# Kernel optimization log

Measured on AMD Instinct MI355X. Metric: run time of the kernel, lower is better.

## Reference

```python
import jax, jax.numpy as jnp
import numpy as np

N_DIS = 5000
N_GEN = 20000
N = N_DIS + N_GEN
E = 400000
N_MIRNA = 2000
EMB = 128
HID = 64


def setup_inputs() -> dict:
    key = jax.random.key(0)
    ks = jax.random.split(key, 20)
    def g(k, shape, scale=0.05):
        return jax.random.normal(k, shape, dtype=jnp.float32) * scale
    return {
        'd_features': g(ks[0], (N_DIS, 383), 1.0),
        'g_features': g(ks[1], (N_GEN, 4395), 1.0),
        'miRNA_dis': jax.random.uniform(ks[2], (N_MIRNA, N_DIS), dtype=jnp.float32),
        'gene_dis': jax.random.uniform(ks[3], (N_GEN, N_DIS), dtype=jnp.float32),
        'Wd': g(ks[4], (383, EMB)),
        'bd': jnp.zeros((EMB,), jnp.float32),
        'Wg': g(ks[5], (4395, EMB)),
        'bg': jnp.zeros((EMB,), jnp.float32),
        'W1': g(ks[6], (N_MIRNA, EMB)),
        'W4': g(ks[7], (N_DIS, EMB)),
        'Ws1': g(ks[8], (EMB, HID)),
        'Wn1': g(ks[9], (EMB, HID)),
        'b1': jnp.zeros((HID,), jnp.float32),
        'Ws2': g(ks[10], (HID, HID)),
        'Wn2': g(ks[11], (HID, HID)),
        'b2': jnp.zeros((HID,), jnp.float32),
        'src': jax.random.randint(ks[12], (E,), 0, N, dtype=jnp.int32),
        'dst': jax.random.randint(ks[13], (E,), 0, N, dtype=jnp.int32),
    }


def _sage_mean(h, src, dst, Ws, Wn, b):
    # DGL SAGEConv 'mean': fc_self(h) + fc_neigh(mean over in-neighbors) + bias
    msg = h[src]                                            # [E, d] gather
    agg = jax.ops.segment_sum(msg, dst, num_segments=N)     # [N, d] scatter-add
    deg = jax.ops.segment_sum(jnp.ones((dst.shape[0],), h.dtype), dst, num_segments=N)
    neigh = agg / jnp.maximum(deg, 1.0)[:, None]            # mean (zero-deg -> 0)
    return h @ Ws + neigh @ Wn + b


def reference(d_features, g_features, miRNA_dis, gene_dis, Wd, bd, Wg, bg,
              W1, W4, Ws1, Wn1, b1, Ws2, Wn2, b2, src, dst):
    # CrossCompressUnit outputs used by forward: A2 = M1^T W1, B1 = M2 W4
    A2 = miRNA_dis.T @ W1          # [N_DIS, EMB]
    B1 = gene_dis @ W4             # [N_GEN, EMB]
    # Node embeddings (dropout is identity at inference; torch.no_grad block)
    h_dis = 0.9 * (d_features @ Wd + bd) + 0.1 * A2   # [N_DIS, EMB]
    h_gen = 0.9 * (g_features @ Wg + bg) + 0.1 * B1   # [N_GEN, EMB]
    h = jnp.concatenate([h_dis, h_gen], axis=0)        # [N, EMB]
    h = _sage_mean(h, src, dst, Ws1, Wn1, b1)          # [N, 64]
    h = jax.nn.relu(h)
    h = _sage_mean(h, src, dst, Ws2, Wn2, b2)          # [N, 64]
    return h
```

## Files before the change

### kernel.cpp

```cpp
#include <hip/hip_runtime.h>

#define NDIS 5000
#define NGEN 20000
#define NTOT 25000
#define EDG  400000

typedef __attribute__((ext_vector_type(8))) short short8;
typedef __attribute__((ext_vector_type(4))) float f32x4;
typedef __attribute__((ext_vector_type(4), aligned(4))) float f32x4u;
typedef __attribute__((ext_vector_type(4))) unsigned int uint4v;
typedef __attribute__((ext_vector_type(2))) unsigned int uint2v;
typedef __attribute__((ext_vector_type(2), aligned(4))) unsigned int uint2a;

constexpr size_t AL(size_t x) { return (x + 255) & ~(size_t)255; }
constexpr size_t OFF_H0   = 0;
constexpr size_t OFF_PQ   = AL(OFF_H0  + (size_t)NTOT * 128 * 4);
constexpr size_t OFF_H1   = AL(OFF_PQ  + (size_t)NTOT * 128 * 4);
constexpr size_t OFF_DEG  = AL(OFF_H1  + (size_t)NTOT * 128 * 4);
constexpr size_t OFF_RS   = AL(OFF_DEG + (size_t)NTOT * 4);
constexpr size_t OFF_CUR  = AL(OFF_RS  + (size_t)(NTOT + 1) * 4);
constexpr size_t OFF_ESRC = AL(OFF_CUR + (size_t)NTOT * 4);
constexpr size_t OFF_MIT  = AL(OFF_ESRC + (size_t)EDG * 4);
constexpr size_t OFF_BDIS = AL(OFF_MIT + (size_t)5000 * 2048 * 2);
constexpr size_t OFF_BGEN = AL(OFF_BDIS + (size_t)8 * 76 * 512 * 2);
constexpr size_t OFF_BS1  = AL(OFF_BGEN + (size_t)8 * 300 * 512 * 2);
constexpr size_t OFF_BS2  = AL(OFF_BS1 + (size_t)8 * 4 * 512 * 2);
constexpr size_t OFF_PD   = AL(OFF_BS2 + (size_t)8 * 4 * 512 * 2);
constexpr size_t OFF_PG   = AL(OFF_PD + (size_t)5 * NDIS * 128 * 4);

__device__ __forceinline__ ushort f2bf(float f) {
    unsigned u = __float_as_uint(f);
    u += 0x7fffu + ((u >> 16) & 1u);
    return (ushort)(u >> 16);
}

__device__ __forceinline__ unsigned cvtpk(float a, float b) {
    unsigned r;
    asm("v_cvt_pk_bf16_f32 %0, %1, %2" : "=v"(r) : "v"(a), "v"(b));
    return r;
}

__device__ __forceinline__ void MFMA(f32x4& d, short8 a, short8 b) {
    asm volatile("v_mfma_f32_16x16x32_bf16 %0, %1, %2, %0"
                 : "+v"(d) : "v"(a), "v"(b));
}

struct TcvtIns { const float* p[9]; };

__global__ __launch_bounds__(256) void k_tcvt_multi(TcvtIns ins, char* ws,
                                                    const int* __restrict__ dst,
                                                    int* __restrict__ deg)
{
    constexpr int   TR[9]   = {383, 2000, 4395, 5000, 2000, 128, 128, 64, 64};
    constexpr int   TC[9]   = {128, 128, 128, 128, 5000, 64, 64, 64, 64};
    constexpr int   TKT[9]  = {76, 76, 300, 300, 2048 , 4, 4, 4, 4};
    constexpr int   TKO[9]  = {0, 12, 0, 140, 0, 0, 0, 0, 0};
    constexpr int   TRP[9]  = {384, 2048, 4480, 5120, 2048, 128, 128, 128, 128};
    constexpr int   TNOFF[9]= {0, 0, 0, 0, 0, 0, 64, 0, 64};
    constexpr int   TMODE[9]= {1, 1, 1, 1, 0, 1, 1, 1, 1};
    constexpr float TSC[9]  = {0.9f, 0.1f, 0.9f, 0.1f, 1.f, 1.f, 1.f, 1.f, 1.f};
    constexpr size_t TOUT[9]= {OFF_BDIS, OFF_BDIS, OFF_BGEN, OFF_BGEN, OFF_MIT,
                               OFF_BS1, OFF_BS1, OFF_BS2, OFF_BS2};
    constexpr int TNBX[9]   = {4, 4, 4, 4, 157, 2, 2, 2, 2};
    constexpr int PRE[10]   = {0, 48, 304, 864, 1504, 11552, 11560, 11568, 11576, 11584};

    int bid = blockIdx.x;
    if (bid >= 11584) {
        int e = (bid - 11584) * 256 + threadIdx.x;
        if (e < EDG) atomicAdd(&deg[dst[e]], 1);
        return;
    }
    int d = 0;
#pragma unroll
    for (int q = 1; q < 9; ++q) if (bid >= PRE[q]) d = q;
    int local = bid - PRE[d];
    int bx = local % TNBX[d], by = local / TNBX[d];
    const int R = TR[d], C = TC[d], KT = TKT[d], KO = TKO[d];
    const int Rp = TRP[d], noff = TNOFF[d];
    const float scale = TSC[d];
    const float* in = ins.p[d];
    ushort* out = (ushort*)(ws + TOUT[d]);

    __shared__ float t[32][33];
    int tx = threadIdx.x & 31, ty = threadIdx.x >> 5;
    int c0 = bx * 32, r0 = by * 32;
#pragma unroll
    for (int j = 0; j < 4; ++j) {
        int r = r0 + ty + j * 8, c = c0 + tx;
        t[ty + j * 8][tx] = (r < R && c < C) ? in[(size_t)r * C + c] : 0.f;
    }
    __syncthreads();
#pragma unroll
    for (int j = 0; j < 4; ++j) {
        int c = c0 + ty + j * 8, r = r0 + tx;
        if (c >= C || r >= Rp) continue;
        ushort bv = f2bf(scale * t[tx][ty + j * 8]);
        if (TMODE[d] == 0) {
            out[(size_t)c * KT + r] = bv;
        } else {
            int n = noff + c, k = r;
            out[(size_t)((n >> 4) * KT + KO + (k >> 5)) * 512 +
                ((k >> 3) & 3) * 128 + (n & 15) * 8 + (k & 7)] = bv;
        }
    }
}

template<int A2MODE, bool PARTIAL>
__global__ __launch_bounds__(256, 2) void gemm_st(
    const float* __restrict__ A1, int lda1, int K1, int nst1,
    const void* __restrict__ A2v, int lda2, int K2, int nst2,
    const ushort* __restrict__ Bf, int KT,
    float* __restrict__ C, int M, const float* __restrict__ bias)
{
    __shared__ ushort lds0[64 * 128];
    __shared__ ushort lds1[64 * 128];
    const int tid  = threadIdx.x;
    const int lane = tid & 63;
    const int w    = tid >> 6;
    const int fr = lane & 15, kq = lane >> 4;
    const int bm0 = blockIdx.x * 64;

    const int NSTT = nst1 + nst2;
    const int per = (NSTT + gridDim.y - 1) / gridDim.y;
    const int s0 = blockIdx.y * per;
    const int s1 = min(NSTT, s0 + per);
    const int NT = s1 - s0;
    if (NT <= 0) return;

    f32x4 acc[4][2];
#pragma unroll
    for (int i = 0; i < 4; ++i) { acc[i][0] = {0.f,0.f,0.f,0.f}; acc[i][1] = {0.f,0.f,0.f,0.f}; }

    uint4v faA[8], faB[8];
    short8 Breg0[4][2], Breg1[4][2];

    const int srow = w * 16 + (lane >> 5);
    const int scol = lane & 31;

    auto issueA = [&](int stg, uint4v* fa) {
        const bool r1 = (A2MODE == 0) || (stg < nst1);
#pragma unroll
        for (int i = 0; i < 8; ++i) {
            int r = bm0 + srow + i * 2;
            if (r > M - 1) r = M - 1;
            if (r1) {
                const int kb = stg << 7;
                const int k = kb + scol * 4;
                const float* p = A1 + (size_t)r * lda1 + k;
                if (kb + 128 <= K1) {
                    fa[i] = __builtin_bit_cast(uint4v, *(const f32x4u*)p);
                } else {
                    f32x4 v;
#pragma unroll
                    for (int e = 0; e < 4; ++e) v[e] = (k + e < K1) ? p[e] : 0.f;
                    fa[i] = __builtin_bit_cast(uint4v, v);
                }
            } else if (A2MODE == 1) {
                const int kb = (stg - nst1) << 7;
                const int kc = kb + scol * 4;
                const float* p = (const float*)A2v + (size_t)r * lda2 + kc;
                if (kb + 128 <= K2) {
                    fa[i] = __builtin_bit_cast(uint4v, *(const f32x4u*)p);
                } else {
                    f32x4 v;
#pragma unroll
                    for (int e = 0; e < 4; ++e) v[e] = (kc + e < K2) ? p[e] : 0.f;
                    fa[i] = __builtin_bit_cast(uint4v, v);
                }
            } else {
                const int kc = ((stg - nst1) << 7) + scol * 4;
                uint2a v = *(const uint2a*)((const ushort*)A2v + (size_t)r * lda2 + kc);
                fa[i][0] = v[0]; fa[i][1] = v[1];
            }
        }
    };
    auto issueB = [&](int stg, short8 (*BR)[2]) {
#pragma unroll
        for (int ks = 0; ks < 4; ++ks)
#pragma unroll
            for (int nf = 0; nf < 2; ++nf)
                BR[ks][nf] = *(const short8*)(
                    Bf + (size_t)((w * 2 + nf) * KT + stg * 4 + ks) * 512 + lane * 8);
    };
    auto writeT = [&](int stg, const uint4v* fa, ushort* buf) {
        const bool cvt = (A2MODE != 2) || (stg < nst1);
        const int G = scol >> 1, h = lane & 1;
#pragma unroll
        for (int i = 0; i < 8; ++i) {
            int r = srow + i * 2;
            const size_t off = (size_t)r * 256 + ((G ^ (r & 7)) << 4) + h * 8;
            uint2v d;
            if (cvt) {
                f32x4 v = __builtin_bit_cast(f32x4, fa[i]);
                d[0] = cvtpk(v[0], v[1]);
                d[1] = cvtpk(v[2], v[3]);
            } else {
                d[0] = fa[i][0]; d[1] = fa[i][1];
            }
            *(uint2v*)((char*)buf + off) = d;
        }
    };

#define PHASE(T, BR, LDSC, FAW, LDSW)                                        \
    {                                                                        \
        const int x7 = fr & 7;                                               \
        _Pragma("unroll")                                                    \
        for (int ks = 0; ks < 4; ++ks) {                                     \
            short8 af[4];                                                    \
            _Pragma("unroll")                                                \
            for (int mf = 0; mf < 4; ++mf)                                   \
                af[mf] = *(const short8*)&LDSC[fr * 128 + mf * 2048 +        \
                                              (((ks * 4 + kq) ^ x7) << 3)];  \
            _Pragma("unroll")                                                \
            for (int mf = 0; mf < 4; ++mf) {                                 \
                MFMA(acc[mf][0], af[mf], BR[ks][0]);                         \
                MFMA(acc[mf][1], af[mf], BR[ks][1]);                         \
            }                                                                \
        }                                                                    \
        if ((T) + 2 < NT) issueB(s0 + (T) + 2, BR);                          \
        __builtin_amdgcn_s_barrier();                                        \
        if ((T) + 1 < NT) {                                                  \
            writeT(s0 + (T) + 1, FAW, LDSW);                                 \
            if ((T) + 3 < NT) issueA(s0 + (T) + 3, FAW);                     \
            asm volatile("s_waitcnt lgkmcnt(0)" ::: "memory");               \
            __builtin_amdgcn_s_barrier();                                    \
        }                                                                    \
    }

    issueA(s0, faA); issueB(s0, Breg0);
    if (NT > 1) { issueA(s0 + 1, faB); issueB(s0 + 1, Breg1); }
    writeT(s0, faA, lds0);
    if (NT > 2) issueA(s0 + 2, faA);
    asm volatile("s_waitcnt lgkmcnt(0)" ::: "memory");
    __builtin_amdgcn_s_barrier();

    for (int t = 0; t < NT; t += 2) {
        PHASE(t, Breg0, lds0, faB, lds1);
        if (t + 1 < NT) PHASE(t + 1, Breg1, lds1, faA, lds0);
    }
#undef PHASE

    asm volatile("s_nop 7\n\ts_nop 7\n\ts_nop 7" ::: "memory");
    float* Cs = PARTIAL ? (C + (size_t)blockIdx.y * ((size_t)M * 128)) : C;
#pragma unroll
    for (int mf = 0; mf < 4; ++mf)
#pragma unroll
        for (int nf = 0; nf < 2; ++nf)
#pragma unroll
            for (int r = 0; r < 4; ++r) {
                int row = bm0 + mf * 16 + kq * 4 + r;
                if (row < M) {
                    int col = w * 32 + nf * 16 + fr;
                    if (PARTIAL) {
                        Cs[(size_t)row * 128 + col] = acc[mf][nf][r];
                    } else {
                        float v = acc[mf][nf][r];
                        if (col < 64) v += bias[col];
                        Cs[(size_t)row * 128 + col] = v;
                    }
                }
            }
}

__global__ __launch_bounds__(256) void k_reduce(
    const float* __restrict__ Pd, const float* __restrict__ Pg,
    const float* __restrict__ bd, const float* __restrict__ bg,
    float* __restrict__ h0)
{
    int i = blockIdx.x * 256 + threadIdx.x;
    if (i >= NTOT * 128) return;
    int row = i >> 7, c = i & 127;
    float v;
    if (row < NDIS) {
        v = 0.9f * bd[c];
#pragma unroll
        for (int s = 0; s < 5; ++s) v += Pd[(size_t)s * NDIS * 128 + i];
    } else {
        v = 0.9f * bg[c];
        int j = i - NDIS * 128;
#pragma unroll
        for (int s = 0; s < 4; ++s) v += Pg[(size_t)s * NGEN * 128 + j];
    }
    h0[i] = v;
}

__global__ __launch_bounds__(1024) void k_scan(const int* __restrict__ deg,
                                               int* __restrict__ row_start,
                                               int* __restrict__ cursor, int n) {
    __shared__ int wsum[16];
    __shared__ int carry_s;
    int t = threadIdx.x;
    int lane = t & 63, wid = t >> 6;
    if (t == 0) { carry_s = 0; row_start[0] = 0; }
    __syncthreads();
    for (int base = 0; base < n; base += 1024) {
        int i = base + t;
        int v = (i < n) ? deg[i] : 0;
        int x = v;
#pragma unroll
        for (int off = 1; off < 64; off <<= 1) {
            int y = __shfl_up(x, off, 64);
            if (lane >= off) x += y;
        }
        if (lane == 63) wsum[wid] = x;
        __syncthreads();
        if (wid == 0) {
            int s = (lane < 16) ? wsum[lane] : 0;
#pragma unroll
            for (int off = 1; off < 16; off <<= 1) {
                int y = __shfl_up(s, off, 64);
                if (lane >= off) s += y;
            }
            if (lane < 16) wsum[lane] = s;
        }
        __syncthreads();
        int pre = (wid > 0 ? wsum[wid - 1] : 0) + carry_s;
        int incl = x + pre;
        if (i < n) { row_start[i + 1] = incl; cursor[i] = incl - v; }
        __syncthreads();
        if (t == 1023) carry_s = incl;
        __syncthreads();
    }
}

__global__ void k_fill(const int* __restrict__ src, const int* __restrict__ dst,
                       int* __restrict__ cursor, int* __restrict__ esrc, int E) {
    int e = blockIdx.x * blockDim.x + threadIdx.x;
    if (e < E) {
        int pos = atomicAdd(&cursor[dst[e]], 1);
        esrc[pos] = src[e];
    }
}

__global__ __launch_bounds__(64) void k_agg(const float* __restrict__ PQ,
                                            const int* __restrict__ rs,
                                            const int* __restrict__ esrc,
                                            float* __restrict__ out, int ldout, int relu)
{
    int n = blockIdx.x, t = threadIdx.x;
    int s0 = rs[n], s1 = rs[n + 1];
    float a0 = 0.f, a1 = 0.f, a2 = 0.f, a3 = 0.f;
    int i = s0;
    for (; i + 4 <= s1; i += 4) {
        int e0 = esrc[i], e1 = esrc[i + 1], e2 = esrc[i + 2], e3 = esrc[i + 3];
        a0 += PQ[(size_t)e0 * 128 + 64 + t];
        a1 += PQ[(size_t)e1 * 128 + 64 + t];
        a2 += PQ[(size_t)e2 * 128 + 64 + t];
        a3 += PQ[(size_t)e3 * 128 + 64 + t];
    }
    for (; i < s1; ++i) a0 += PQ[(size_t)esrc[i] * 128 + 64 + t];
    float s = (a0 + a1) + (a2 + a3);
    float dg = (float)(s1 - s0);
    s /= fmaxf(dg, 1.f);
    float v = PQ[(size_t)n * 128 + t] + s;
    if (relu) v = fmaxf(v, 0.f);
    out[(size_t)n * ldout + t] = v;
}

extern "C" void kernel_launch(void* const* d_in, const int* in_sizes, int n_in,
                              void* d_out, int out_size, void* d_ws, size_t ws_size,
                              hipStream_t stream)
{
    const float* d_features = (const float*)d_in[0];
    const float* g_features = (const float*)d_in[1];
    const float* miRNA_dis  = (const float*)d_in[2];
    const float* gene_dis   = (const float*)d_in[3];
    const float* Wd  = (const float*)d_in[4];
    const float* bd  = (const float*)d_in[5];
    const float* Wg  = (const float*)d_in[6];
    const float* bg  = (const float*)d_in[7];
    const float* W1  = (const float*)d_in[8];
    const float* W4  = (const float*)d_in[9];
    const float* Ws1 = (const float*)d_in[10];
    const float* Wn1 = (const float*)d_in[11];
    const float* b1  = (const float*)d_in[12];
    const float* Ws2 = (const float*)d_in[13];
    const float* Wn2 = (const float*)d_in[14];
    const float* b2  = (const float*)d_in[15];
    const int* src = (const int*)d_in[16];
    const int* dst = (const int*)d_in[17];
    (void)in_sizes; (void)n_in; (void)out_size; (void)ws_size;

    char* ws = (char*)d_ws;
    float*  h0   = (float*)(ws + OFF_H0);
    float*  PQ   = (float*)(ws + OFF_PQ);
    float*  h1   = (float*)(ws + OFF_H1);
    int*    deg  = (int*)(ws + OFF_DEG);
    int*    rs   = (int*)(ws + OFF_RS);
    int*    cur  = (int*)(ws + OFF_CUR);
    int*    esrc = (int*)(ws + OFF_ESRC);
    ushort* miT  = (ushort*)(ws + OFF_MIT);
    ushort* Bdis = (ushort*)(ws + OFF_BDIS);
    ushort* Bgen = (ushort*)(ws + OFF_BGEN);
    ushort* Bs1  = (ushort*)(ws + OFF_BS1);
    ushort* Bs2  = (ushort*)(ws + OFF_BS2);
    float*  Pd   = (float*)(ws + OFF_PD);
    float*  Pg   = (float*)(ws + OFF_PG);

    hipMemsetAsync(deg, 0, (size_t)NTOT * 4, stream);
    hipMemsetAsync(h1, 0, (size_t)NTOT * 128 * 4, stream);

    TcvtIns ins;
    ins.p[0] = Wd;  ins.p[1] = W1;  ins.p[2] = Wg;  ins.p[3] = W4;
    ins.p[4] = miRNA_dis; ins.p[5] = Ws1; ins.p[6] = Wn1; ins.p[7] = Ws2; ins.p[8] = Wn2;
    k_tcvt_multi<<<11584 + 1563, 256, 0, stream>>>(ins, ws, dst, deg);

    k_scan<<<1, 1024, 0, stream>>>(deg, rs, cur, NTOT);
    k_fill<<<(EDG + 255) / 256, 256, 0, stream>>>(src, dst, cur, esrc, EDG);

    gemm_st<2, true><<<dim3(79, 5), 256, 0, stream>>>(
        d_features, 383, 383, 3,
        miT, 2048, 2048, 16, Bdis, 76, Pd, NDIS, nullptr);
    gemm_st<1, true><<<dim3(313, 4), 256, 0, stream>>>(
        g_features, 4395, 4395, 35,
        gene_dis, 5000, 5000, 40, Bgen, 300, Pg, NGEN, nullptr);
    k_reduce<<<(NTOT * 128 + 255) / 256, 256, 0, stream>>>(Pd, Pg, bd, bg, h0);

    gemm_st<0, false><<<dim3(391, 1), 256, 0, stream>>>(
        h0, 128, 128, 1, nullptr, 0, 0, 0, Bs1, 4, PQ, NTOT, b1);
    k_agg<<<NTOT, 64, 0, stream>>>(PQ, rs, esrc, h1, 128, 1);

    gemm_st<0, false><<<dim3(391, 1), 256, 0, stream>>>(
        h1, 128, 128, 1, nullptr, 0, 0, 0, Bs2, 4, PQ, NTOT, b2);
    k_agg<<<NTOT, 64, 0, stream>>>(PQ, rs, esrc, (float*)d_out, 64, 0);
}
```

Baseline: 379.5 us.

## Fuse embedding GEMMs into one launch, parallelize degree scan, shrink h1 width

Merges the disease and gene embedding GEMMs into a single launch that dispatches per block through a runtime op descriptor. The gene GEMM's K split grows from four to five partials, and the reduce kernel reads five. The single-block degree scan is replaced by a three-kernel multi-block scan. The hidden buffer h1 is stored at width 64, which removes its memset and halves the second GEMM's K. The goal is less tail idle time and lower launch and serial overhead. The cost is that templated A-mode branches become runtime branches, which may add register pressure.

Result: slower. 423.1 us (+11.5%).

```diff
diff --git a/kernel.cpp b/kernel.cpp
--- a/kernel.cpp
+++ b/kernel.cpp
@@ -16,10 +16,13 @@
 constexpr size_t OFF_H0   = 0;
 constexpr size_t OFF_PQ   = AL(OFF_H0  + (size_t)NTOT * 128 * 4);
 constexpr size_t OFF_H1   = AL(OFF_PQ  + (size_t)NTOT * 128 * 4);
-constexpr size_t OFF_DEG  = AL(OFF_H1  + (size_t)NTOT * 128 * 4);
+constexpr size_t OFF_DEG  = AL(OFF_H1  + (size_t)NTOT * 64 * 4);
 constexpr size_t OFF_RS   = AL(OFF_DEG + (size_t)NTOT * 4);
 constexpr size_t OFF_CUR  = AL(OFF_RS  + (size_t)(NTOT + 1) * 4);
-constexpr size_t OFF_ESRC = AL(OFF_CUR + (size_t)NTOT * 4);
+constexpr size_t OFF_TMP  = AL(OFF_CUR + (size_t)NTOT * 4);
+constexpr size_t OFF_BSUM = AL(OFF_TMP + (size_t)NTOT * 4);
+constexpr size_t OFF_BOFF = AL(OFF_BSUM + 64 * 4);
+constexpr size_t OFF_ESRC = AL(OFF_BOFF + 64 * 4);
 constexpr size_t OFF_MIT  = AL(OFF_ESRC + (size_t)EDG * 4);
 constexpr size_t OFF_BDIS = AL(OFF_MIT + (size_t)5000 * 2048 * 2);
 constexpr size_t OFF_BGEN = AL(OFF_BDIS + (size_t)8 * 76 * 512 * 2);
@@ -105,20 +108,34 @@
     }
 }
 
-template<int A2MODE, bool PARTIAL>
+struct EmbOp {
+    const float* A1; int lda1, K1, nst1;
+    const void* A2v; int lda2, K2, nst2;
+    const ushort* Bf; int KT; float* C; int M; int a2mode;
+};
+
+template<bool PARTIAL>
 __global__ __launch_bounds__(256, 2) void gemm_st(
-    const float* __restrict__ A1, int lda1, int K1, int nst1,
-    const void* __restrict__ A2v, int lda2, int K2, int nst2,
-    const ushort* __restrict__ Bf, int KT,
-    float* __restrict__ C, int M, const float* __restrict__ bias)
+    EmbOp opg, EmbOp opd, int bxsplit, const float* __restrict__ bias)
 {
+    const bool isg = (int)blockIdx.x < bxsplit;
+    const EmbOp op = isg ? opg : opd;
+    const float* __restrict__ A1 = op.A1;
+    const int lda1 = op.lda1, K1 = op.K1, nst1 = op.nst1;
+    const void* __restrict__ A2v = op.A2v;
+    const int lda2 = op.lda2, K2 = op.K2, nst2 = op.nst2;
+    const ushort* __restrict__ Bf = op.Bf;
+    const int KT = op.KT, M = op.M, a2mode = op.a2mode;
+    float* __restrict__ C = op.C;
+
     __shared__ ushort lds0[64 * 128];
     __shared__ ushort lds1[64 * 128];
     const int tid  = threadIdx.x;
     const int lane = tid & 63;
     const int w    = tid >> 6;
     const int fr = lane & 15, kq = lane >> 4;
-    const int bm0 = blockIdx.x * 64;
+    const int bm0 = (isg ? blockIdx.x : (blockIdx.x - bxsplit)) * 64;
+    if (bm0 >= M + 63) return;
 
     const int NSTT = nst1 + nst2;
     const int per = (NSTT + gridDim.y - 1) / gridDim.y;
@@ -138,7 +155,7 @@
     const int scol = lane & 31;
 
     auto issueA = [&](int stg, uint4v* fa) {
-        const bool r1 = (A2MODE == 0) || (stg < nst1);
+        const bool r1 = (a2mode == 0) || (stg < nst1);
 #pragma unroll
         for (int i = 0; i < 8; ++i) {
             int r = bm0 + srow + i * 2;
@@ -155,7 +172,7 @@
                     for (int e = 0; e < 4; ++e) v[e] = (k + e < K1) ? p[e] : 0.f;
                     fa[i] = __builtin_bit_cast(uint4v, v);
                 }
-            } else if (A2MODE == 1) {
+            } else if (a2mode == 1) {
                 const int kb = (stg - nst1) << 7;
                 const int kc = kb + scol * 4;
                 const float* p = (const float*)A2v + (size_t)r * lda2 + kc;
@@ -183,7 +200,7 @@
                     Bf + (size_t)((w * 2 + nf) * KT + stg * 4 + ks) * 512 + lane * 8);
     };
     auto writeT = [&](int stg, const uint4v* fa, ushort* buf) {
-        const bool cvt = (A2MODE != 2) || (stg < nst1);
+        const bool cvt = (a2mode != 2) || (stg < nst1);
         const int G = scol >> 1, h = lane & 1;
 #pragma unroll
         for (int i = 0; i < 8; ++i) {
@@ -279,47 +296,64 @@
         v = 0.9f * bg[c];
         int j = i - NDIS * 128;
 #pragma unroll
-        for (int s = 0; s < 4; ++s) v += Pg[(size_t)s * NGEN * 128 + j];
+        for (int s = 0; s < 5; ++s) v += Pg[(size_t)s * NGEN * 128 + j];
     }
     h0[i] = v;
 }
 
-__global__ __launch_bounds__(1024) void k_scan(const int* __restrict__ deg,
-                                               int* __restrict__ row_start,
-                                               int* __restrict__ cursor, int n) {
+__global__ __launch_bounds__(1024) void k_scan1(const int* __restrict__ deg,
+                                                int* __restrict__ tmp,
+                                                int* __restrict__ bsum, int n) {
     __shared__ int wsum[16];
-    __shared__ int carry_s;
+    int t = threadIdx.x, lane = t & 63, wid = t >> 6;
+    int i = blockIdx.x * 1024 + t;
+    int v = (i < n) ? deg[i] : 0;
+    int x = v;
+#pragma unroll
+    for (int off = 1; off < 64; off <<= 1) {
+        int y = __shfl_up(x, off, 64);
+        if (lane >= off) x += y;
+    }
+    if (lane == 63) wsum[wid] = x;
+    __syncthreads();
+    if (wid == 0) {
+        int s = (lane < 16) ? wsum[lane] : 0;
+#pragma unroll
+        for (int off = 1; off < 16; off <<= 1) {
+            int y = __shfl_up(s, off, 64);
+            if (lane >= off) s += y;
+        }
+        if (lane < 16) wsum[lane] = s;
+    }
+    __syncthreads();
+    int incl = x + (wid > 0 ? wsum[wid - 1] : 0);
+    if (i < n) tmp[i] = incl;
+    if (t == 1023) bsum[blockIdx.x] = incl;
+}
+
+__global__ void k_scan2(const int* __restrict__ bsum, int* __restrict__ boff, int nb) {
     int t = threadIdx.x;
-    int lane = t & 63, wid = t >> 6;
-    if (t == 0) { carry_s = 0; row_start[0] = 0; }
-    __syncthreads();
-    for (int base = 0; base < n; base += 1024) {
-        int i = base + t;
-        int v = (i < n) ? deg[i] : 0;
-        int x = v;
-#pragma unroll
-        for (int off = 1; off < 64; off <<= 1) {
-            int y = __shfl_up(x, off, 64);
-            if (lane >= off) x += y;
-        }
-        if (lane == 63) wsum[wid] = x;
-        __syncthreads();
-        if (wid == 0) {
-            int s = (lane < 16) ? wsum[lane] : 0;
-#pragma unroll
-            for (int off = 1; off < 16; off <<= 1) {
-                int y = __shfl_up(s, off, 64);
-                if (lane >= off) s += y;
-            }
-            if (lane < 16) wsum[lane] = s;
-        }
-        __syncthreads();
-        int pre = (wid > 0 ? wsum[wid - 1] : 0) + carry_s;
-        int incl = x + pre;
-        if (i < n) { row_start[i + 1] = incl; cursor[i] = incl - v; }
-        __syncthreads();
-        if (t == 1023) carry_s = incl;
-        __syncthreads();
+    int v = (t < nb) ? bsum[t] : 0;
+    int x = v;
+#pragma unroll
+    for (int off = 1; off < 64; off <<= 1) {
+        int y = __shfl_up(x, off, 64);
+        if (t >= off) x += y;
+    }
+    if (t < nb) boff[t] = x - v;
+}
+
+__global__ __launch_bounds__(1024) void k_scan3(const int* __restrict__ deg,
+                                                const int* __restrict__ tmp,
+                                                const int* __restrict__ boff,
+                                                int* __restrict__ rs,
+                                                int* __restrict__ cursor, int n) {
+    int i = blockIdx.x * 1024 + threadIdx.x;
+    if (i == 0) rs[0] = 0;
+    if (i < n) {
+        int v = tmp[i] + boff[blockIdx.x];
+        rs[i + 1] = v;
+        cursor[i] = v - deg[i];
     }
 }
 
@@ -388,6 +422,9 @@
     int*    deg  = (int*)(ws + OFF_DEG);
     int*    rs   = (int*)(ws + OFF_RS);
     int*    cur  = (int*)(ws + OFF_CUR);
+    int*    tmp  = (int*)(ws + OFF_TMP);
+    int*    bsum = (int*)(ws + OFF_BSUM);
+    int*    boff = (int*)(ws + OFF_BOFF);
     int*    esrc = (int*)(ws + OFF_ESRC);
     ushort* miT  = (ushort*)(ws + OFF_MIT);
     ushort* Bdis = (ushort*)(ws + OFF_BDIS);
@@ -398,29 +435,29 @@
     float*  Pg   = (float*)(ws + OFF_PG);
 
     hipMemsetAsync(deg, 0, (size_t)NTOT * 4, stream);
-    hipMemsetAsync(h1, 0, (size_t)NTOT * 128 * 4, stream);
 
     TcvtIns ins;
     ins.p[0] = Wd;  ins.p[1] = W1;  ins.p[2] = Wg;  ins.p[3] = W4;
     ins.p[4] = miRNA_dis; ins.p[5] = Ws1; ins.p[6] = Wn1; ins.p[7] = Ws2; ins.p[8] = Wn2;
     k_tcvt_multi<<<11584 + 1563, 256, 0, stream>>>(ins, ws, dst, deg);
 
-    k_scan<<<1, 1024, 0, stream>>>(deg, rs, cur, NTOT);
+    k_scan1<<<25, 1024, 0, stream>>>(deg, tmp, bsum, NTOT);
+    k_scan2<<<1, 64, 0, stream>>>(bsum, boff, 25);
+    k_scan3<<<25, 1024, 0, stream>>>(deg, tmp, boff, rs, cur, NTOT);
     k_fill<<<(EDG + 255) / 256, 256, 0, stream>>>(src, dst, cur, esrc, EDG);
 
-    gemm_st<2, true><<<dim3(79, 5), 256, 0, stream>>>(
-        d_features, 383, 383, 3,
-        miT, 2048, 2048, 16, Bdis, 76, Pd, NDIS, nullptr);
-    gemm_st<1, true><<<dim3(313, 4), 256, 0, stream>>>(
-        g_features, 4395, 4395, 35,
-        gene_dis, 5000, 5000, 40, Bgen, 300, Pg, NGEN, nullptr);
+    EmbOp opg = {g_features, 4395, 4395, 35, gene_dis, 5000, 5000, 40,
+                 Bgen, 300, Pg, NGEN, 1};
+    EmbOp opd = {d_features, 383, 383, 3, miT, 2048, 2048, 16,
+                 Bdis, 76, Pd, NDIS, 2};
+    gemm_st<true><<<dim3(392, 5), 256, 0, stream>>>(opg, opd, 313, nullptr);
     k_reduce<<<(NTOT * 128 + 255) / 256, 256, 0, stream>>>(Pd, Pg, bd, bg, h0);
 
-    gemm_st<0, false><<<dim3(391, 1), 256, 0, stream>>>(
-        h0, 128, 128, 1, nullptr, 0, 0, 0, Bs1, 4, PQ, NTOT, b1);
-    k_agg<<<NTOT, 64, 0, stream>>>(PQ, rs, esrc, h1, 128, 1);
-
-    gemm_st<0, false><<<dim3(391, 1), 256, 0, stream>>>(
-        h1, 128, 128, 1, nullptr, 0, 0, 0, Bs2, 4, PQ, NTOT, b2);
+    EmbOp ops1 = {h0, 128, 128, 1, nullptr, 0, 0, 0, Bs1, 4, PQ, NTOT, 0};
+    gemm_st<false><<<dim3(391, 1), 256, 0, stream>>>(ops1, ops1, 391, b1);
+    k_agg<<<NTOT, 64, 0, stream>>>(PQ, rs, esrc, h1, 64, 1);
+
+    EmbOp ops2 = {h1, 64, 64, 1, nullptr, 0, 0, 0, Bs2, 4, PQ, NTOT, 0};
+    gemm_st<false><<<dim3(391, 1), 256, 0, stream>>>(ops2, ops2, 391, b2);
     k_agg<<<NTOT, 64, 0, stream>>>(PQ, rs, esrc, (float*)d_out, 64, 0);
 }
```
